# Performance work log

Measured on AMD Instinct MI355X. Metric: run time of the kernel, lower is better.

The kernel has to match this reference:

```python
import jax, jax.numpy as jnp
import numpy as np

EMBED = 1024
HEADS = 16
HEAD_DIM = EMBED // HEADS
RANK = 8
ALPHA = 16.0
SCALING = ALPHA / RANK  # 2.0
B, T = 2, 2048


def setup_inputs() -> dict:
    key = jax.random.key(0)
    ks = jax.random.split(key, 12)
    d = {
        'x': jax.random.normal(ks[0], (B, T, EMBED), dtype=jnp.float32),
        'Wq': jax.random.normal(ks[1], (EMBED, EMBED), dtype=jnp.float32),
        'Aq': jax.random.normal(ks[2], (EMBED, RANK), dtype=jnp.float32) * 0.01,
        'Bq': jnp.zeros((RANK, EMBED), dtype=jnp.float32),
        'Wk': jax.random.normal(ks[3], (EMBED, EMBED), dtype=jnp.float32),
        'Ak': jax.random.normal(ks[4], (EMBED, RANK), dtype=jnp.float32) * 0.01,
        'Bk': jnp.zeros((RANK, EMBED), dtype=jnp.float32),
        'Wv': jax.random.normal(ks[5], (EMBED, EMBED), dtype=jnp.float32),
        'Av': jax.random.normal(ks[6], (EMBED, RANK), dtype=jnp.float32) * 0.01,
        'Bv': jnp.zeros((RANK, EMBED), dtype=jnp.float32),
        'Wo': jax.random.normal(ks[7], (EMBED, EMBED), dtype=jnp.float32) * (1.0 / np.sqrt(EMBED)),
        'bo': jnp.zeros((EMBED,), dtype=jnp.float32),
    }
    return d


def _lora_linear(x, W, A, Bm):
    # torch F.linear(x, W) == x @ W.T ; LoRA bypass: x @ A @ B * scaling
    base = jnp.einsum('btc,oc->bto', x, W)
    lora = (x @ A) @ Bm * SCALING
    return base + lora


def reference(x, Wq, Aq, Bq, Wk, Ak, Bk, Wv, Av, Bv, Wo, bo):
    b, t, c = x.shape
    q = _lora_linear(x, Wq, Aq, Bq).reshape(b, t, HEADS, HEAD_DIM).transpose(0, 2, 1, 3)
    k = _lora_linear(x, Wk, Ak, Bk).reshape(b, t, HEADS, HEAD_DIM).transpose(0, 2, 1, 3)
    v = _lora_linear(x, Wv, Av, Bv).reshape(b, t, HEADS, HEAD_DIM).transpose(0, 2, 1, 3)
    scores = jnp.einsum('bhqd,bhkd->bhqk', q, k) / np.sqrt(HEAD_DIM).astype(np.float32)
    attn = jax.nn.softmax(scores, axis=-1)
    ctx = jnp.einsum('bhqk,bhkd->bhqd', attn, v)  # [B,H,T,D]
    out = ctx.transpose(0, 2, 1, 3).reshape(b, t, c)
    return jnp.einsum('btc,oc->bto', out, Wo) + bo
```

## Files before the change

### kernel.cpp

```cpp
#include <hip/hip_runtime.h>
#include <hip/hip_bf16.h>
#include <math.h>

#define EMBED 1024
#define HEADS 16
#define HDIM 64
#define RANK 8
#define BB 2
#define TT 2048
#define MTOT (BB*TT)
#define BH (BB*HEADS)

typedef __attribute__((ext_vector_type(8))) short bf16x8;
typedef __attribute__((ext_vector_type(4))) float f32x4;
typedef unsigned short u16;
typedef unsigned int u32;

__device__ __forceinline__ u16 f2bf(float f){
  unsigned u = __float_as_uint(f);
  u += 0x7FFF + ((u >> 16) & 1);
  return (u16)(u >> 16);
}
__device__ __forceinline__ float bf2f(u16 h){ return __uint_as_float(((unsigned)h) << 16); }

__device__ __forceinline__ u32 cvtpk(float lo, float hi){
  u32 r;
  asm("v_cvt_pk_bf16_f32 %0, %1, %2" : "=v"(r) : "v"(lo), "v"(hi));
  return r;
}

__device__ __forceinline__ float fexp2(float x){
  float r;
  asm("v_exp_f32 %0, %1" : "=v"(r) : "v"(x));
  return r;
}

__device__ __forceinline__ void stage16(const void* g, void* l){
  __builtin_amdgcn_global_load_lds((const __attribute__((address_space(1))) unsigned int*)g,
                                   (__attribute__((address_space(3))) unsigned int*)l, 16, 0, 0);
}

__global__ void split_x_kernel(const float* __restrict__ x, u16* __restrict__ xhi, u16* __restrict__ xlo){
  int i = blockIdx.x * 256 + threadIdx.x;
  float v = x[i];
  u16 h = f2bf(v);
  xhi[i] = h;
  xlo[i] = f2bf(v - bf2f(h));
}

__global__ void prep_weights_kernel(const float* __restrict__ W0, const float* __restrict__ W1,
                                    const float* __restrict__ W2, const float* __restrict__ W3,
                                    const float* __restrict__ A0, const float* __restrict__ A1,
                                    const float* __restrict__ A2,
                                    const float* __restrict__ B0, const float* __restrict__ B1,
                                    const float* __restrict__ B2,
                                    u16* __restrict__ whi, u16* __restrict__ wlo,
                                    u16* __restrict__ wob){
  int i = blockIdx.x * 256 + threadIdx.x;
  int y = blockIdx.y;
  if (y == 3){ wob[i] = f2bf(W3[i]); return; }
  const float* W = (y == 0) ? W0 : (y == 1) ? W1 : W2;
  const float* A = (y == 0) ? A0 : (y == 1) ? A1 : A2;
  const float* Bm = (y == 0) ? B0 : (y == 1) ? B1 : B2;
  int o = i >> 10, c = i & 1023;
  float s = 0.f;
#pragma unroll
  for (int r = 0; r < RANK; ++r) s += A[c*RANK+r] * Bm[r*EMBED+o];
  float v = W[i] + 2.0f * s;
  u16 h = f2bf(v);
  size_t off = (size_t)y * 1048576 + i;
  whi[off] = h;
  wlo[off] = f2bf(v - bf2f(h));
}

__device__ __forceinline__ int swz4(int row){ return (row ^ (row >> 2)) & 3; }

__global__ __launch_bounds__(256)
void qkv_gemm(const u16* __restrict__ Ahi, const u16* __restrict__ Alo,
              const u16* __restrict__ Bhi, const u16* __restrict__ Blo,
              u16* __restrict__ qhi, u16* __restrict__ qlo,
              u16* __restrict__ khi, u16* __restrict__ klo,
              u16* __restrict__ vt)
{
  __shared__ __align__(16) u16 Ah[128*32], Bh[128*32], Al[128*32], Bl[128*32];
  const int t = threadIdx.x, lane = t & 63, w = t >> 6;
  const int wr = w >> 1, wc = w & 1;
  const int fr = lane & 15, fk = lane >> 4;
  const int m0 = blockIdx.y * 128, n0 = blockIdx.x * 128;
  const bool full = (n0 < 2048);

  f32x4 acc[4][4];
#pragma unroll
  for (int i = 0; i < 4; ++i)
#pragma unroll
    for (int j = 0; j < 4; ++j) acc[i][j] = (f32x4){0.f,0.f,0.f,0.f};

  for (int k0 = 0; k0 < EMBED; k0 += 32){
    __syncthreads();
#pragma unroll
    for (int cc = 0; cc < 2; ++cc){
      int cb = w*128 + cc*64;
      int chunk = cb + lane;
      int row = chunk >> 2, slot = chunk & 3;
      int sl = slot ^ swz4(row);
      stage16(Ahi + (size_t)(m0+row)*EMBED + k0 + sl*8, Ah + cb*8);
      stage16(Bhi + (size_t)(n0+row)*EMBED + k0 + sl*8, Bh + cb*8);
      if (full){
        stage16(Alo + (size_t)(m0+row)*EMBED + k0 + sl*8, Al + cb*8);
        stage16(Blo + (size_t)(n0+row)*EMBED + k0 + sl*8, Bl + cb*8);
      }
    }
    __syncthreads();

    bf16x8 ah[4], bh[4], al[4], bl[4];
#pragma unroll
    for (int i = 0; i < 4; ++i){
      int ra = wr*64 + i*16 + fr;
      int oa = ra*32 + (fk ^ swz4(ra))*8;
      ah[i] = *(const bf16x8*)&Ah[oa];
      if (full) al[i] = *(const bf16x8*)&Al[oa];
      int rb = wc*64 + i*16 + fr;
      int ob = rb*32 + (fk ^ swz4(rb))*8;
      bh[i] = *(const bf16x8*)&Bh[ob];
      if (full) bl[i] = *(const bf16x8*)&Bl[ob];
    }
#pragma unroll
    for (int i = 0; i < 4; ++i)
#pragma unroll
      for (int j = 0; j < 4; ++j){
        acc[i][j] = __builtin_amdgcn_mfma_f32_16x16x32_bf16(ah[i], bh[j], acc[i][j], 0,0,0);
        if (full){
          acc[i][j] = __builtin_amdgcn_mfma_f32_16x16x32_bf16(ah[i], bl[j], acc[i][j], 0,0,0);
          acc[i][j] = __builtin_amdgcn_mfma_f32_16x16x32_bf16(al[i], bh[j], acc[i][j], 0,0,0);
        }
      }
  }

  const int mat = (n0 + wc*64) >> 10;
  const float QSCALE = 0.125f * 1.44269504089f;
#pragma unroll
  for (int i = 0; i < 4; ++i)
#pragma unroll
    for (int j = 0; j < 4; ++j)
#pragma unroll
      for (int r = 0; r < 4; ++r){
        int gm = m0 + wr*64 + i*16 + fk*4 + r;
        int gn = n0 + wc*64 + j*16 + fr;
        int col = gn & 1023;
        float v = acc[i][j][r];
        int b = gm >> 11, tt2 = gm & 2047, h = col >> 6, d = col & 63;
        if (mat == 2){
          vt[((size_t)(b*HEADS + h)*HDIM + d)*TT + tt2] = f2bf(v);
        } else {
          if (mat == 0) v *= QSCALE;
          size_t idx = ((size_t)(b*HEADS + h)*TT + tt2)*HDIM + d;
          u16 hi = f2bf(v);
          u16 lo = f2bf(v - bf2f(hi));
          if (mat == 0){ qhi[idx] = hi; qlo[idx] = lo; }
          else         { khi[idx] = hi; klo[idx] = lo; }
        }
      }
}

__global__ __launch_bounds__(256)
void attn_mfma(const u16* __restrict__ Qhi, const u16* __restrict__ Qlo,
               const u16* __restrict__ Khi, const u16* __restrict__ Klo,
               const u16* __restrict__ Vt,  u16* __restrict__ ctx)
{
  __shared__ __align__(16) u16 smem[16384];
  u16* Kh = smem;
  u16* Kl = smem + 4096;
  u16* Vs = smem + 8192;
  u16* Ps = smem + 12288;
  const int t = threadIdx.x, lane = t & 63, w = t >> 6;
  const int fr = lane & 15, fk = lane >> 4;
  const int bh = blockIdx.y, q0 = blockIdx.x * 64;
  const size_t kbase = (size_t)bh * TT * HDIM;
  const size_t vbase = (size_t)bh * HDIM * TT;

#pragma unroll
  for (int cc = 0; cc < 2; ++cc){
    int cb = w*128 + cc*64;
    int chunk = cb + lane;
    int row = chunk >> 3, slot = chunk & 7;
    int sl = slot ^ (row & 7);
    stage16(Qhi + kbase + (size_t)(q0+row)*HDIM + sl*8, Kh + cb*8);
    stage16(Qlo + kbase + (size_t)(q0+row)*HDIM + sl*8, Kl + cb*8);
  }
  __syncthreads();
  bf16x8 qh[2], ql[2];
#pragma unroll
  for (int ks = 0; ks < 2; ++ks){
    int row = w*16 + fr;
    int off = row*64 + ((ks*4 + fk) ^ (row & 7))*8;
    qh[ks] = *(const bf16x8*)&Kh[off];
    ql[ks] = *(const bf16x8*)&Kl[off];
  }

  float mi = -1e30f, li = 0.f;
  f32x4 oacc[4];
#pragma unroll
  for (int n = 0; n < 4; ++n) oacc[n] = (f32x4){0.f,0.f,0.f,0.f};

  for (int kt = 0; kt < TT/64; ++kt){
    int kv0 = kt * 64;
    __syncthreads();
#pragma unroll
    for (int cc = 0; cc < 2; ++cc){
      int cb = w*128 + cc*64;
      int chunk = cb + lane;
      int row = chunk >> 3, slot = chunk & 7;
      int sl = slot ^ (row & 7);
      stage16(Khi + kbase + (size_t)(kv0+row)*HDIM + sl*8, Kh + cb*8);
      stage16(Klo + kbase + (size_t)(kv0+row)*HDIM + sl*8, Kl + cb*8);
      stage16(Vt  + vbase + (size_t)row*TT + kv0 + sl*8,  Vs + cb*8);
    }
    __syncthreads();

    f32x4 sacc[4];
#pragma unroll
    for (int n = 0; n < 4; ++n) sacc[n] = (f32x4){0.f,0.f,0.f,0.f};
#pragma unroll
    for (int n = 0; n < 4; ++n)
#pragma unroll
      for (int ks = 0; ks < 2; ++ks){
        int row = n*16 + fr;
        int off = row*64 + ((ks*4 + fk) ^ (row & 7))*8;
        bf16x8 kh = *(const bf16x8*)&Kh[off];
        bf16x8 kl = *(const bf16x8*)&Kl[off];
        sacc[n] = __builtin_amdgcn_mfma_f32_16x16x32_bf16(kh, qh[ks], sacc[n], 0,0,0);
        sacc[n] = __builtin_amdgcn_mfma_f32_16x16x32_bf16(kl, qh[ks], sacc[n], 0,0,0);
        sacc[n] = __builtin_amdgcn_mfma_f32_16x16x32_bf16(kh, ql[ks], sacc[n], 0,0,0);
      }

    float mt = fmaxf(fmaxf(sacc[0][0], sacc[0][1]), fmaxf(sacc[0][2], sacc[0][3]));
#pragma unroll
    for (int n = 1; n < 4; ++n)
      mt = fmaxf(mt, fmaxf(fmaxf(sacc[n][0], sacc[n][1]), fmaxf(sacc[n][2], sacc[n][3])));
    mt = fmaxf(mt, __shfl_xor(mt, 16));
    mt = fmaxf(mt, __shfl_xor(mt, 32));

    if (__any(mt > mi + 11.54f)){
      float mn = fmaxf(mi, mt);
      float sc = fexp2(mi - mn);
      mi = mn;
      li *= sc;
      float sct[4];
#pragma unroll
      for (int r = 0; r < 4; ++r) sct[r] = __shfl(sc, fk*4 + r);
#pragma unroll
      for (int n = 0; n < 4; ++n)
#pragma unroll
        for (int r = 0; r < 4; ++r) oacc[n][r] *= sct[r];
    }

    float rs = 0.f;
#pragma unroll
    for (int n = 0; n < 4; ++n)
#pragma unroll
      for (int r = 0; r < 4; ++r){
        float p = fexp2(sacc[n][r] - mi);
        sacc[n][r] = p;
        rs += p;
      }
    rs += __shfl_xor(rs, 16);
    rs += __shfl_xor(rs, 32);
    li += rs;

#pragma unroll
    for (int n = 0; n < 4; ++n){
      u32 u0 = cvtpk(sacc[n][0], sacc[n][1]);
      u32 u1 = cvtpk(sacc[n][2], sacc[n][3]);
      int slot = n*2 + (fk >> 1);
      int idx = w*1024 + fr*64 + (slot ^ (fr & 7))*8 + (fk & 1)*4;
      uint2 pk; pk.x = u0; pk.y = u1;
      *(uint2*)&Ps[idx] = pk;
    }

#pragma unroll
    for (int ks = 0; ks < 2; ++ks){
      bf16x8 pa = *(const bf16x8*)&Ps[w*1024 + fr*64 + ((ks*4 + fk) ^ (fr & 7))*8];
#pragma unroll
      for (int n = 0; n < 4; ++n){
        int row = n*16 + fr;
        bf16x8 bv = *(const bf16x8*)&Vs[row*64 + ((ks*4 + fk) ^ (row & 7))*8];
        oacc[n] = __builtin_amdgcn_mfma_f32_16x16x32_bf16(pa, bv, oacc[n], 0,0,0);
      }
    }
  }

  float inv = 1.f / li;
  float invt[4];
#pragma unroll
  for (int r = 0; r < 4; ++r) invt[r] = __shfl(inv, fk*4 + r);

  int b = bh >> 4, h = bh & 15;
#pragma unroll
  for (int r = 0; r < 4; ++r){
    int q = q0 + w*16 + fk*4 + r;
#pragma unroll
    for (int n = 0; n < 4; ++n){
      int d = n*16 + fr;
      ctx[((size_t)(b*TT + q))*EMBED + h*HDIM + d] = f2bf(oacc[n][r]*invt[r]);
    }
  }
}

__global__ __launch_bounds__(256)
void outproj_gemm(const u16* __restrict__ Ab, const u16* __restrict__ Bb,
                  const float* __restrict__ bias, float* __restrict__ C)
{
  __shared__ __align__(16) u16 Ah[128*32], Bh[128*32];
  const int t = threadIdx.x, lane = t & 63, w = t >> 6;
  const int wr = w >> 1, wc = w & 1;
  const int fr = lane & 15, fk = lane >> 4;
  const int m0 = blockIdx.y * 128, n0 = blockIdx.x * 128;

  f32x4 acc[4][4];
#pragma unroll
  for (int i = 0; i < 4; ++i)
#pragma unroll
    for (int j = 0; j < 4; ++j) acc[i][j] = (f32x4){0.f,0.f,0.f,0.f};

  for (int k0 = 0; k0 < EMBED; k0 += 32){
    __syncthreads();
#pragma unroll
    for (int cc = 0; cc < 2; ++cc){
      int cb = w*128 + cc*64;
      int chunk = cb + lane;
      int row = chunk >> 2, slot = chunk & 3;
      int sl = slot ^ swz4(row);
      stage16(Ab + (size_t)(m0+row)*EMBED + k0 + sl*8, Ah + cb*8);
      stage16(Bb + (size_t)(n0+row)*EMBED + k0 + sl*8, Bh + cb*8);
    }
    __syncthreads();

    bf16x8 ah[4], bh[4];
#pragma unroll
    for (int i = 0; i < 4; ++i){
      int ra = wr*64 + i*16 + fr;
      ah[i] = *(const bf16x8*)&Ah[ra*32 + (fk ^ swz4(ra))*8];
      int rb = wc*64 + i*16 + fr;
      bh[i] = *(const bf16x8*)&Bh[rb*32 + (fk ^ swz4(rb))*8];
    }
#pragma unroll
    for (int i = 0; i < 4; ++i)
#pragma unroll
      for (int j = 0; j < 4; ++j)
        acc[i][j] = __builtin_amdgcn_mfma_f32_16x16x32_bf16(ah[i], bh[j], acc[i][j], 0,0,0);
  }

#pragma unroll
  for (int i = 0; i < 4; ++i)
#pragma unroll
    for (int j = 0; j < 4; ++j)
#pragma unroll
      for (int r = 0; r < 4; ++r){
        int gm = m0 + wr*64 + i*16 + fk*4 + r;
        int gn = n0 + wc*64 + j*16 + fr;
        C[(size_t)gm*EMBED + gn] = acc[i][j][r] + bias[gn];
      }
}

extern "C" void kernel_launch(void* const* d_in, const int* in_sizes, int n_in,
                              void* d_out, int out_size, void* d_ws, size_t ws_size,
                              hipStream_t stream) {
  const float* x  = (const float*)d_in[0];
  const float* Wq = (const float*)d_in[1];
  const float* Aq = (const float*)d_in[2];
  const float* Bq = (const float*)d_in[3];
  const float* Wk = (const float*)d_in[4];
  const float* Ak = (const float*)d_in[5];
  const float* Bk = (const float*)d_in[6];
  const float* Wv = (const float*)d_in[7];
  const float* Av = (const float*)d_in[8];
  const float* Bv = (const float*)d_in[9];
  const float* Wo = (const float*)d_in[10];
  const float* bo = (const float*)d_in[11];
  float* out = (float*)d_out;

  char* ws = (char*)d_ws;
  const size_t MB = 1u << 20;
  u16* xhi  = (u16*)(ws + 0*MB);
  u16* xlo  = (u16*)(ws + 8*MB);
  u16* whi  = (u16*)(ws + 16*MB);
  u16* wlo  = (u16*)(ws + 22*MB);
  u16* wob  = (u16*)(ws + 28*MB);
  u16* qhi  = (u16*)(ws + 30*MB);
  u16* qlo  = (u16*)(ws + 38*MB);
  u16* khi  = (u16*)(ws + 46*MB);
  u16* klo  = (u16*)(ws + 54*MB);
  u16* vt   = (u16*)(ws + 62*MB);
  u16* ctx  = (u16*)(ws + 0*MB);

  dim3 blk(256);
  split_x_kernel<<<dim3(MTOT*EMBED/256), blk, 0, stream>>>(x, xhi, xlo);
  prep_weights_kernel<<<dim3(4096, 4), blk, 0, stream>>>(Wq, Wk, Wv, Wo, Aq, Ak, Av,
                                                         Bq, Bk, Bv, whi, wlo, wob);

  qkv_gemm<<<dim3(3*EMBED/128, MTOT/128), blk, 0, stream>>>(xhi, xlo, whi, wlo,
                                                            qhi, qlo, khi, klo, vt);

  attn_mfma<<<dim3(TT/64, BH), blk, 0, stream>>>(qhi, qlo, khi, klo, vt, ctx);

  outproj_gemm<<<dim3(EMBED/128, MTOT/128), blk, 0, stream>>>(ctx, wob, bo, out);
}
```

Baseline: 291.8 us.

## Hoist attention address math, add MFMA priority hints, shrink outproj tile

The attention kernel now computes LDS offsets and global staging pointers once before the KV loop and advances the pointers by increments, which cuts integer work inside the loop. It also wraps the MFMA sections in s_setprio and asks launch_bounds for 4 blocks per CU. Separately, the output projection drops to 64x128 tiles, doubling the grid for better CU coverage at the cost of less reuse per tile. Keeping the offsets in registers may raise register pressure against the occupancy target.

```diff
diff --git a/kernel.cpp b/kernel.cpp
--- a/kernel.cpp
+++ b/kernel.cpp
@@ -162,7 +162,7 @@
       }
 }
 
-__global__ __launch_bounds__(256)
+__global__ __launch_bounds__(256, 4)
 void attn_mfma(const u16* __restrict__ Qhi, const u16* __restrict__ Qlo,
                const u16* __restrict__ Khi, const u16* __restrict__ Klo,
                const u16* __restrict__ Vt,  u16* __restrict__ ctx)
@@ -197,41 +197,63 @@
     ql[ks] = *(const bf16x8*)&Kl[off];
   }
 
+  int offK[4][2], idxP[4], offP[2];
+#pragma unroll
+  for (int n = 0; n < 4; ++n){
+#pragma unroll
+    for (int ks = 0; ks < 2; ++ks){
+      int row = n*16 + fr;
+      offK[n][ks] = row*64 + ((ks*4 + fk) ^ (row & 7))*8;
+    }
+    idxP[n] = w*1024 + fr*64 + ((n*2 + (fk >> 1)) ^ (fr & 7))*8 + (fk & 1)*4;
+  }
+#pragma unroll
+  for (int ks = 0; ks < 2; ++ks)
+    offP[ks] = w*1024 + fr*64 + ((ks*4 + fk) ^ (fr & 7))*8;
+
+  int sdst[2];
+  const u16 *sKh[2], *sKl[2], *sV[2];
+#pragma unroll
+  for (int cc = 0; cc < 2; ++cc){
+    int chunk = w*128 + cc*64 + lane;
+    int row = chunk >> 3, slot = chunk & 7;
+    int sl = slot ^ (row & 7);
+    sdst[cc] = chunk*8;
+    sKh[cc] = Khi + kbase + (size_t)row*HDIM + sl*8;
+    sKl[cc] = Klo + kbase + (size_t)row*HDIM + sl*8;
+    sV [cc] = Vt  + vbase + (size_t)row*TT  + sl*8;
+  }
+
   float mi = -1e30f, li = 0.f;
   f32x4 oacc[4];
 #pragma unroll
   for (int n = 0; n < 4; ++n) oacc[n] = (f32x4){0.f,0.f,0.f,0.f};
 
   for (int kt = 0; kt < TT/64; ++kt){
-    int kv0 = kt * 64;
     __syncthreads();
 #pragma unroll
     for (int cc = 0; cc < 2; ++cc){
-      int cb = w*128 + cc*64;
-      int chunk = cb + lane;
-      int row = chunk >> 3, slot = chunk & 7;
-      int sl = slot ^ (row & 7);
-      stage16(Khi + kbase + (size_t)(kv0+row)*HDIM + sl*8, Kh + cb*8);
-      stage16(Klo + kbase + (size_t)(kv0+row)*HDIM + sl*8, Kl + cb*8);
-      stage16(Vt  + vbase + (size_t)row*TT + kv0 + sl*8,  Vs + cb*8);
+      stage16(sKh[cc], Kh + sdst[cc]);  sKh[cc] += 64*HDIM;
+      stage16(sKl[cc], Kl + sdst[cc]);  sKl[cc] += 64*HDIM;
+      stage16(sV [cc], Vs + sdst[cc]);  sV [cc] += 64;
     }
     __syncthreads();
 
     f32x4 sacc[4];
 #pragma unroll
     for (int n = 0; n < 4; ++n) sacc[n] = (f32x4){0.f,0.f,0.f,0.f};
+    __builtin_amdgcn_s_setprio(1);
 #pragma unroll
     for (int n = 0; n < 4; ++n)
 #pragma unroll
       for (int ks = 0; ks < 2; ++ks){
-        int row = n*16 + fr;
-        int off = row*64 + ((ks*4 + fk) ^ (row & 7))*8;
-        bf16x8 kh = *(const bf16x8*)&Kh[off];
-        bf16x8 kl = *(const bf16x8*)&Kl[off];
+        bf16x8 kh = *(const bf16x8*)&Kh[offK[n][ks]];
+        bf16x8 kl = *(const bf16x8*)&Kl[offK[n][ks]];
         sacc[n] = __builtin_amdgcn_mfma_f32_16x16x32_bf16(kh, qh[ks], sacc[n], 0,0,0);
         sacc[n] = __builtin_amdgcn_mfma_f32_16x16x32_bf16(kl, qh[ks], sacc[n], 0,0,0);
         sacc[n] = __builtin_amdgcn_mfma_f32_16x16x32_bf16(kh, ql[ks], sacc[n], 0,0,0);
       }
+    __builtin_amdgcn_s_setprio(0);
 
     float mt = fmaxf(fmaxf(sacc[0][0], sacc[0][1]), fmaxf(sacc[0][2], sacc[0][3]));
 #pragma unroll
@@ -271,22 +293,21 @@
     for (int n = 0; n < 4; ++n){
       u32 u0 = cvtpk(sacc[n][0], sacc[n][1]);
       u32 u1 = cvtpk(sacc[n][2], sacc[n][3]);
-      int slot = n*2 + (fk >> 1);
-      int idx = w*1024 + fr*64 + (slot ^ (fr & 7))*8 + (fk & 1)*4;
       uint2 pk; pk.x = u0; pk.y = u1;
-      *(uint2*)&Ps[idx] = pk;
-    }
-
+      *(uint2*)&Ps[idxP[n]] = pk;
+    }
+
+    __builtin_amdgcn_s_setprio(1);
 #pragma unroll
     for (int ks = 0; ks < 2; ++ks){
-      bf16x8 pa = *(const bf16x8*)&Ps[w*1024 + fr*64 + ((ks*4 + fk) ^ (fr & 7))*8];
+      bf16x8 pa = *(const bf16x8*)&Ps[offP[ks]];
 #pragma unroll
       for (int n = 0; n < 4; ++n){
-        int row = n*16 + fr;
-        bf16x8 bv = *(const bf16x8*)&Vs[row*64 + ((ks*4 + fk) ^ (row & 7))*8];
+        bf16x8 bv = *(const bf16x8*)&Vs[offK[n][ks]];
         oacc[n] = __builtin_amdgcn_mfma_f32_16x16x32_bf16(pa, bv, oacc[n], 0,0,0);
       }
     }
+    __builtin_amdgcn_s_setprio(0);
   }
 
   float inv = 1.f / li;
@@ -310,54 +331,60 @@
 void outproj_gemm(const u16* __restrict__ Ab, const u16* __restrict__ Bb,
                   const float* __restrict__ bias, float* __restrict__ C)
 {
-  __shared__ __align__(16) u16 Ah[128*32], Bh[128*32];
+  __shared__ __align__(16) u16 Ah[64*32], Bh[128*32];
   const int t = threadIdx.x, lane = t & 63, w = t >> 6;
-  const int wr = w >> 1, wc = w & 1;
   const int fr = lane & 15, fk = lane >> 4;
-  const int m0 = blockIdx.y * 128, n0 = blockIdx.x * 128;
-
-  f32x4 acc[4][4];
+  const int m0 = blockIdx.y * 64, n0 = blockIdx.x * 128;
+
+  f32x4 acc[4][2];
 #pragma unroll
   for (int i = 0; i < 4; ++i)
 #pragma unroll
-    for (int j = 0; j < 4; ++j) acc[i][j] = (f32x4){0.f,0.f,0.f,0.f};
+    for (int j = 0; j < 2; ++j) acc[i][j] = (f32x4){0.f,0.f,0.f,0.f};
 
   for (int k0 = 0; k0 < EMBED; k0 += 32){
     __syncthreads();
-#pragma unroll
-    for (int cc = 0; cc < 2; ++cc){
-      int cb = w*128 + cc*64;
-      int chunk = cb + lane;
-      int row = chunk >> 2, slot = chunk & 3;
+    {
+      int s = w*64 + lane;
+      int row = s >> 2, slot = s & 3;
       int sl = slot ^ swz4(row);
-      stage16(Ab + (size_t)(m0+row)*EMBED + k0 + sl*8, Ah + cb*8);
-      stage16(Bb + (size_t)(n0+row)*EMBED + k0 + sl*8, Bh + cb*8);
-    }
-    __syncthreads();
-
-    bf16x8 ah[4], bh[4];
+      stage16(Ab + (size_t)(m0+row)*EMBED + k0 + sl*8, Ah + s*8);
+    }
+#pragma unroll
+    for (int c = 0; c < 2; ++c){
+      int s = (w*2 + c)*64 + lane;
+      int row = s >> 2, slot = s & 3;
+      int sl = slot ^ swz4(row);
+      stage16(Bb + (size_t)(n0+row)*EMBED + k0 + sl*8, Bh + s*8);
+    }
+    __syncthreads();
+
+    bf16x8 ah[4], bh[2];
 #pragma unroll
     for (int i = 0; i < 4; ++i){
-      int ra = wr*64 + i*16 + fr;
+      int ra = i*16 + fr;
       ah[i] = *(const bf16x8*)&Ah[ra*32 + (fk ^ swz4(ra))*8];
-      int rb = wc*64 + i*16 + fr;
-      bh[i] = *(const bf16x8*)&Bh[rb*32 + (fk ^ swz4(rb))*8];
+    }
+#pragma unroll
+    for (int j = 0; j < 2; ++j){
+      int rb = w*32 + j*16 + fr;
+      bh[j] = *(const bf16x8*)&Bh[rb*32 + (fk ^ swz4(rb))*8];
     }
 #pragma unroll
     for (int i = 0; i < 4; ++i)
 #pragma unroll
-      for (int j = 0; j < 4; ++j)
+      for (int j = 0; j < 2; ++j)
         acc[i][j] = __builtin_amdgcn_mfma_f32_16x16x32_bf16(ah[i], bh[j], acc[i][j], 0,0,0);
   }
 
 #pragma unroll
   for (int i = 0; i < 4; ++i)
 #pragma unroll
-    for (int j = 0; j < 4; ++j)
+    for (int j = 0; j < 2; ++j)
 #pragma unroll
       for (int r = 0; r < 4; ++r){
-        int gm = m0 + wr*64 + i*16 + fk*4 + r;
-        int gn = n0 + wc*64 + j*16 + fr;
+        int gm = m0 + i*16 + fk*4 + r;
+        int gn = n0 + w*32 + j*16 + fr;
         C[(size_t)gm*EMBED + gn] = acc[i][j][r] + bias[gn];
       }
 }
@@ -403,5 +430,5 @@
 
   attn_mfma<<<dim3(TT/64, BH), blk, 0, stream>>>(qhi, qlo, khi, klo, vt, ctx);
 
-  outproj_gemm<<<dim3(EMBED/128, MTOT/128), blk, 0, stream>>>(ctx, wob, bo, out);
-}
+  outproj_gemm<<<dim3(EMBED/128, MTOT/64), blk, 0, stream>>>(ctx, wob, bo, out);
+}
```

Result: faster. 279.3 us (-4.3%).
